# Kernel optimization log

Hardware: AMD Instinct MI355X
Metric: run time of the kernel (lower is better)

The kernel has to match this reference:

```python
import jax, jax.numpy as jnp
import numpy as np

B, L = 2, 4096
D_MODEL, STATE, CONV, EXPAND, HEADDIM = 1024, 128, 4, 2, 64
D_INNER = EXPAND * D_MODEL            # 2048
NHEADS = D_INNER // HEADDIM           # 32
CONV_DIM = D_INNER + 2 * STATE        # x, B, C channels (ngroups=1)
D_IN_PROJ = 2 * D_INNER + 2 * STATE + NHEADS
MLP_INNER = 4096
EPS = 1e-5

def _silu(x):
    return x * jax.nn.sigmoid(x)

def _rmsnorm_prenorm(x, res, w):
    # rmsnorm_fn(prenorm=True): residual update then RMSNorm of the residual
    res = x + res
    normed = res * jax.lax.rsqrt(jnp.mean(res * res, axis=-1, keepdims=True) + EPS)
    return normed * w, res

def _mamba2(x, in_proj_w, conv_w, conv_b, dt_bias, A_log, D_param, out_proj_w):
    b, l, _ = x.shape
    zxbcdt = x @ in_proj_w.T                                   # (b,l,D_IN_PROJ)
    z, xBC, dt = jnp.split(zxbcdt, [D_INNER, D_INNER + CONV_DIM], axis=-1)
    # causal depthwise conv1d + silu over [x, B, C]
    xp = jnp.pad(xBC, ((0, 0), (CONV - 1, 0), (0, 0)))
    conv = sum(xp[:, j:j + l, :] * conv_w[None, None, :, j] for j in range(CONV)) + conv_b
    xBC = _silu(conv)
    xh, Bm, Cm = jnp.split(xBC, [D_INNER, D_INNER + STATE], axis=-1)
    xh = xh.reshape(b, l, NHEADS, HEADDIM)                     # (b,l,h,p)
    dt = jax.nn.softplus(dt + dt_bias)                         # (b,l,h)
    A = -jnp.exp(A_log)                                        # (h,)

    def step(state, inp):
        x_t, B_t, C_t, dt_t = inp                              # (b,h,p),(b,n),(b,n),(b,h)
        dA = jnp.exp(dt_t * A)                                 # (b,h)
        state = state * dA[..., None, None] + jnp.einsum('bh,bhp,bn->bhpn', dt_t, x_t, B_t)
        y_t = jnp.einsum('bhpn,bn->bhp', state, C_t)
        return state, y_t

    xs = (xh.transpose(1, 0, 2, 3), Bm.transpose(1, 0, 2), Cm.transpose(1, 0, 2), dt.transpose(1, 0, 2))
    state0 = jnp.zeros((b, NHEADS, HEADDIM, STATE), dtype=x.dtype)
    _, y = jax.lax.scan(step, state0, xs)                      # y: (l,b,h,p)
    y = y.transpose(1, 0, 2, 3) + D_param[None, None, :, None] * xh
    y = y * _silu(z).reshape(b, l, NHEADS, HEADDIM)            # rmsnorm=False -> gate with silu(z)
    return y.reshape(b, l, D_INNER) @ out_proj_w.T

def _mlp(x, gate_w, up_w, down_w):
    return (_silu(x @ gate_w.T) * (x @ up_w.T)) @ down_w.T

def setup_inputs() -> dict:
    key = jax.random.key(0)
    ks = jax.random.split(key, 12)
    s = 0.02
    return {
        'hidden_states': jax.random.normal(ks[0], (B, L, D_MODEL), jnp.float32),
        'residual': jax.random.normal(ks[1], (B, L, D_MODEL), jnp.float32),
        'ssm_norm_w': jnp.ones((D_MODEL,), jnp.float32),
        'mlp_norm_w': jnp.ones((D_MODEL,), jnp.float32),
        'in_proj_w': jax.random.normal(ks[2], (D_IN_PROJ, D_MODEL), jnp.float32) * s,
        'conv_w': jax.random.normal(ks[3], (CONV_DIM, CONV), jnp.float32) * 0.1,
        'conv_b': jnp.zeros((CONV_DIM,), jnp.float32),
        'dt_bias': jax.random.uniform(ks[4], (NHEADS,), jnp.float32, -4.0, -1.0),
        'A_log': jnp.log(jax.random.uniform(ks[5], (NHEADS,), jnp.float32, 1.0, 16.0)),
        'D_param': jnp.ones((NHEADS,), jnp.float32),
        'out_proj_w': jax.random.normal(ks[6], (D_MODEL, D_INNER), jnp.float32) * s,
        'mlp_gate_w': jax.random.normal(ks[7], (MLP_INNER, D_MODEL), jnp.float32) * s,
        'mlp_up_w': jax.random.normal(ks[8], (MLP_INNER, D_MODEL), jnp.float32) * s,
        'mlp_down_w': jax.random.normal(ks[9], (D_MODEL, MLP_INNER), jnp.float32) * s,
    }

def reference(hidden_states, residual, ssm_norm_w, mlp_norm_w, in_proj_w, conv_w, conv_b,
              dt_bias, A_log, D_param, out_proj_w, mlp_gate_w, mlp_up_w, mlp_down_w):
    h, res = _rmsnorm_prenorm(hidden_states, residual, ssm_norm_w)
    h = _mamba2(h, in_proj_w, conv_w, conv_b, dt_bias, A_log, D_param, out_proj_w)
    h, res = _rmsnorm_prenorm(h, res, mlp_norm_w)
    h = _mlp(h, mlp_gate_w, mlp_up_w, mlp_down_w)
    return h, res
```

## Files before the change

kernel.cpp:

```cpp
#include <hip/hip_runtime.h>

typedef __bf16 bf16x8 __attribute__((ext_vector_type(8)));
typedef float  f32x4  __attribute__((ext_vector_type(4)));

#define GLOAD_LDS16(gp, lp) \
  __builtin_amdgcn_global_load_lds((const __attribute__((address_space(1))) void*)(gp), \
                                   (__attribute__((address_space(3))) void*)(lp), 16, 0, 0)

__device__ __forceinline__ unsigned short f2bf(float f) {
  unsigned u = __float_as_uint(f);
  u += 0x7fffu + ((u >> 16) & 1u);
  return (unsigned short)(u >> 16);
}
__device__ __forceinline__ float bf2f(unsigned short h) {
  return __uint_as_float(((unsigned)h) << 16);
}
__device__ __forceinline__ f32x4 splat4(float v) { f32x4 r = {v, v, v, v}; return r; }

__device__ __forceinline__ f32x4 up4(unsigned lo, unsigned hi) {
  f32x4 r;
  r[0] = __uint_as_float(lo << 16); r[1] = __uint_as_float(lo & 0xffff0000u);
  r[2] = __uint_as_float(hi << 16); r[3] = __uint_as_float(hi & 0xffff0000u);
  return r;
}
__device__ __forceinline__ unsigned pk2(float a, float b) {
  return (unsigned)f2bf(a) | ((unsigned)f2bf(b) << 16);
}

__device__ __forceinline__ void store_out(unsigned short* C, size_t idx, float v) {
  C[idx] = f2bf(v);
}
__device__ __forceinline__ void store_out(float* C, size_t idx, float v) {
  C[idx] = v;
}

__global__ __launch_bounds__(256) void rmsnorm1_kernel(
    const float* __restrict__ hid, const float* __restrict__ resin,
    const float* __restrict__ w, float* __restrict__ resout,
    unsigned short* __restrict__ hout)
{
  const int row = blockIdx.x, t = threadIdx.x;
  const size_t base = (size_t)row * 1024;
  float4 h = ((const float4*)(hid + base))[t];
  float4 r = ((const float4*)(resin + base))[t];
  float4 s; s.x = h.x + r.x; s.y = h.y + r.y; s.z = h.z + r.z; s.w = h.w + r.w;
  float ss = s.x*s.x + s.y*s.y + s.z*s.z + s.w*s.w;
  #pragma unroll
  for (int off = 32; off; off >>= 1) ss += __shfl_down(ss, off, 64);
  __shared__ float red[4];
  if ((t & 63) == 0) red[t >> 6] = ss;
  __syncthreads();
  float tot = red[0] + red[1] + red[2] + red[3];
  float sc = rsqrtf(tot * (1.0f/1024.0f) + 1e-5f);
  ((float4*)(resout + base))[t] = s;
  float4 wv = ((const float4*)w)[t];
  ushort4 o = make_ushort4(f2bf(s.x*sc*wv.x), f2bf(s.y*sc*wv.y),
                           f2bf(s.z*sc*wv.z), f2bf(s.w*sc*wv.w));
  ((ushort4*)(hout + base))[t] = o;
}

__global__ __launch_bounds__(256) void rmsnorm2_kernel(
    const unsigned short* __restrict__ mo, const float* __restrict__ res1,
    const float* __restrict__ w, float* __restrict__ res_out,
    unsigned short* __restrict__ h2)
{
  const int row = blockIdx.x, t = threadIdx.x;
  const size_t base = (size_t)row * 1024;
  float4 r = ((const float4*)(res1 + base))[t];
  ushort4 m = ((const ushort4*)(mo + base))[t];
  float4 s; s.x = r.x + bf2f(m.x); s.y = r.y + bf2f(m.y);
            s.z = r.z + bf2f(m.z); s.w = r.w + bf2f(m.w);
  float ss = s.x*s.x + s.y*s.y + s.z*s.z + s.w*s.w;
  #pragma unroll
  for (int off = 32; off; off >>= 1) ss += __shfl_down(ss, off, 64);
  __shared__ float red[4];
  if ((t & 63) == 0) red[t >> 6] = ss;
  __syncthreads();
  float tot = red[0] + red[1] + red[2] + red[3];
  float sc = rsqrtf(tot * (1.0f/1024.0f) + 1e-5f);
  ((float4*)(res_out + base))[t] = s;
  float4 wv = ((const float4*)w)[t];
  ((ushort4*)(h2 + base))[t] = make_ushort4(f2bf(s.x*sc*wv.x), f2bf(s.y*sc*wv.y),
                                            f2bf(s.z*sc*wv.z), f2bf(s.w*sc*wv.w));
}

__global__ __launch_bounds__(256) void cast_w(
    const float* __restrict__ src, unsigned short* __restrict__ dst,
    int rows, int cols, int prows)
{
  size_t i4 = ((size_t)blockIdx.x * 256 + threadIdx.x) * 4;
  size_t total = (size_t)prows * cols;
  if (i4 >= total) return;
  int r = (int)(i4 / cols);
  ushort4 o;
  if (r < rows) {
    float4 v = *(const float4*)(src + i4);
    o = make_ushort4(f2bf(v.x), f2bf(v.y), f2bf(v.z), f2bf(v.w));
  } else {
    o = make_ushort4(0, 0, 0, 0);
  }
  *(ushort4*)(dst + i4) = o;
}

template <typename OutT, int TN>
__global__ __launch_bounds__(512) void gemm256(
    const unsigned short* __restrict__ A, const unsigned short* __restrict__ W,
    OutT* __restrict__ C, int K, int lda, int ldc, int Nst)
{
  constexpr int NI = TN / 64;
  constexpr int WN = TN / 4;
  constexpr int SB = 2 + TN / 128;
  __shared__ unsigned short As[2][2][8192];
  __shared__ unsigned short Bs[2][2][TN * 32];

  const int gx = gridDim.x, nwg = gx * (int)gridDim.y;
  int lin = blockIdx.y * gx + blockIdx.x;
  {
    const int q = nwg >> 3, r = nwg & 7, xcd = lin & 7, lo = lin >> 3;
    lin = (xcd < r ? xcd * (q + 1) : r * (q + 1) + (xcd - r) * q) + lo;
  }
  const int n0 = (lin % gx) * TN, m0 = (lin / gx) << 8;

  const int t = threadIdx.x, lane = t & 63, w = t >> 6;
  const int wr = w >> 2, wc = w & 3;
  const int fr = lane & 15, fq = lane >> 4;
  const int gsw = ((fq ^ ((fr ^ (fr >> 2)) & 3)) << 3);
  const int srl = t >> 2;
  const int sg  = (t & 3);

  f32x4 acc[8][NI];
  #pragma unroll
  for (int i = 0; i < 8; ++i)
    #pragma unroll
    for (int j = 0; j < NI; ++j) acc[i][j] = splat4(0.f);

  auto stageA = [&](int buf, int ks, int kc) {
    #pragma unroll
    for (int h = 0; h < 2; ++h) {
      const int rl = h * 128 + srl;
      const int swz = (rl ^ (rl >> 2)) & 3;
      const unsigned short* g = A + (size_t)(m0 + rl) * lda + kc + ks * 32 + ((sg ^ swz) << 3);
      GLOAD_LDS16(g, &As[buf][ks][h * 4096 + (w << 9)]);
    }
  };
  auto stageB = [&](int buf, int ks, int kc) {
    #pragma unroll
    for (int h = 0; h < TN / 128; ++h) {
      const int rl = h * 128 + srl;
      const int swz = (rl ^ (rl >> 2)) & 3;
      const unsigned short* g = W + (size_t)(n0 + rl) * (size_t)K + kc + ks * 32 + ((sg ^ swz) << 3);
      GLOAD_LDS16(g, &Bs[buf][ks][h * 4096 + (w << 9)]);
    }
  };

  auto phase = [&](int cb, int ks) {
    bf16x8 af[8], bq[NI];
    #pragma unroll
    for (int mi = 0; mi < 8; ++mi) {
      const int R = wr * 128 + mi * 16 + fr;
      af[mi] = *(const bf16x8*)(&As[cb][ks][R * 32 + gsw]);
    }
    #pragma unroll
    for (int ni = 0; ni < NI; ++ni) {
      const int R = wc * WN + ni * 16 + fr;
      bq[ni] = *(const bf16x8*)(&Bs[cb][ks][R * 32 + gsw]);
    }
    __builtin_amdgcn_s_setprio(1);
    #pragma unroll
    for (int mi = 0; mi < 8; ++mi)
      #pragma unroll
      for (int ni = 0; ni < NI; ++ni)
        acc[mi][ni] = __builtin_amdgcn_mfma_f32_16x16x32_bf16(af[mi], bq[ni], acc[mi][ni], 0, 0, 0);
    __builtin_amdgcn_s_setprio(0);
  };

  stageA(0, 0, 0); stageB(0, 0, 0);
  stageA(0, 1, 0); stageB(0, 1, 0);

  const int NKT = K >> 6;
  for (int kt = 0; kt < NKT; ++kt) {
    const int cb = kt & 1, nb = cb ^ 1;
    const bool pre = (kt + 1 < NKT);
    const int kc = (kt + 1) << 6;
    if (pre) {
      stageA(nb, 0, kc); stageB(nb, 0, kc);
      asm volatile("s_waitcnt vmcnt(%0)" :: "n"(2 * SB) : "memory");
    } else {
      asm volatile("s_waitcnt vmcnt(%0)" :: "n"(SB) : "memory");
    }
    asm volatile("s_barrier" ::: "memory");
    phase(cb, 0);
    asm volatile("s_barrier" ::: "memory");
    if (pre) {
      stageA(nb, 1, kc); stageB(nb, 1, kc);
      asm volatile("s_waitcnt vmcnt(%0)" :: "n"(2 * SB) : "memory");
    } else {
      asm volatile("s_waitcnt vmcnt(0)" ::: "memory");
    }
    asm volatile("s_barrier" ::: "memory");
    phase(cb, 1);
    asm volatile("s_barrier" ::: "memory");
  }

  #pragma unroll
  for (int mi = 0; mi < 8; ++mi)
    #pragma unroll
    for (int ni = 0; ni < NI; ++ni)
      #pragma unroll
      for (int rr = 0; rr < 4; ++rr) {
        const int gm = m0 + wr * 128 + mi * 16 + fq * 4 + rr;
        const int gn = n0 + wc * WN + ni * 16 + fr;
        if (gn < Nst) store_out(C, (size_t)gm * ldc + gn, acc[mi][ni][rr]);
      }
}

__global__ __launch_bounds__(256) void conv_dt_kernel(
    const unsigned short* __restrict__ zx, const float* __restrict__ conv_w,
    const float* __restrict__ conv_b, const float* __restrict__ dt_bias,
    const float* __restrict__ A_log, unsigned short* __restrict__ conv_out,
    float2* __restrict__ dtda)
{
  size_t idx = (size_t)blockIdx.x * 256 + threadIdx.x;
  if (idx >= (size_t)8192 * 2336) return;
  int c = (int)(idx % 2336);
  int row = (int)(idx / 2336);
  int l = row & 4095;
  if (c < 2304) {
    float acc = conv_b[c];
    const float* wp = conv_w + c * 4;
    #pragma unroll
    for (int j = 0; j < 4; j++) {
      int ls = l - 3 + j;
      if (ls >= 0) acc += bf2f(zx[(size_t)(row - 3 + j) * 4480 + 2048 + c]) * wp[j];
    }
    float s = acc / (1.0f + expf(-acc));
    conv_out[(size_t)row * 2304 + c] = f2bf(s);
  } else {
    int h = c - 2304;
    float draw = bf2f(zx[(size_t)row * 4480 + 4352 + h]) + dt_bias[h];
    float sp = (draw > 20.0f) ? draw : log1pf(expf(draw));
    float Ah = -expf(A_log[h]);
    dtda[(size_t)row * 32 + h] = make_float2(sp, expf(sp * Ah));
  }
}


__global__ __launch_bounds__(256) void chunk_state_kernel(
    const unsigned short* __restrict__ convo, const float2* __restrict__ dtda,
    const float* __restrict__ A_log, unsigned short* __restrict__ Sg,
    float* __restrict__ Pend)
{
  __shared__ __align__(16) unsigned short bT[128 * 136];
  __shared__ __align__(16) unsigned short xT[64 * 136];
  __shared__ float wsh[128];
  const int t = threadIdx.x, lane = t & 63, wv = t >> 6;
  const int c = blockIdx.x & 31, h = (blockIdx.x >> 5) & 31, b = (int)(blockIdx.x >> 10);
  const size_t r0 = (size_t)b * 4096 + (size_t)c * 128;

  if (wv == 0) {
    const float A = -expf(A_log[h]);
    const float s0 = dtda[(r0 + 2 * lane) * 32 + h].x;
    const float s1 = dtda[(r0 + 2 * lane + 1) * 32 + h].x;
    const float v1 = s1 * A;
    float ps = s0 * A + v1;
    #pragma unroll
    for (int off = 1; off < 64; off <<= 1) {
      float n = __shfl_up(ps, off, 64);
      if (lane >= off) ps += n;
    }
    const float laQ = __shfl(ps, 63, 64);
    wsh[2 * lane]     = expf(laQ - (ps - v1)) * s0;
    wsh[2 * lane + 1] = expf(laQ - ps) * s1;
    if (lane == 63) Pend[blockIdx.x] = expf(laQ);
  }
  __syncthreads();

  {
    int j = t >> 3;
    const int p0 = (t & 7) << 3;
    #pragma unroll
    for (int it = 0; it < 4; ++it, j += 32) {
      const uint4 v = *(const uint4*)(convo + (r0 + j) * 2304 + h * 64 + p0);
      const float w = wsh[j];
      const unsigned arr[4] = {v.x, v.y, v.z, v.w};
      #pragma unroll
      for (int e = 0; e < 8; ++e) {
        const unsigned short raw = (unsigned short)(arr[e >> 1] >> ((e & 1) * 16));
        xT[(p0 + e) * 136 + j] = f2bf(bf2f(raw) * w);
      }
    }
  }
  {
    int j = t >> 4;
    const int n0 = (t & 15) << 3;
    #pragma unroll
    for (int it = 0; it < 8; ++it, j += 16) {
      const uint4 v = *(const uint4*)(convo + (r0 + j) * 2304 + 2048 + n0);
      const unsigned arr[4] = {v.x, v.y, v.z, v.w};
      #pragma unroll
      for (int e = 0; e < 8; ++e)
        bT[(n0 + e) * 136 + j] = (unsigned short)(arr[e >> 1] >> ((e & 1) * 16));
    }
  }
  __syncthreads();

  const int fr = lane & 15, fq = lane >> 4;
  const int wn = wv << 5;
  f32x4 acc[4][2];
  #pragma unroll
  for (int i = 0; i < 4; ++i)
    #pragma unroll
    for (int j = 0; j < 2; ++j) acc[i][j] = splat4(0.f);

  #pragma unroll
  for (int k0 = 0; k0 < 128; k0 += 32) {
    bf16x8 af[4], bf[2];
    #pragma unroll
    for (int i = 0; i < 4; ++i)
      af[i] = *(const bf16x8*)(xT + (i * 16 + fr) * 136 + fq * 8 + k0);
    #pragma unroll
    for (int j = 0; j < 2; ++j)
      bf[j] = *(const bf16x8*)(bT + (wn + j * 16 + fr) * 136 + fq * 8 + k0);
    #pragma unroll
    for (int i = 0; i < 4; ++i)
      #pragma unroll
      for (int j = 0; j < 2; ++j)
        acc[i][j] = __builtin_amdgcn_mfma_f32_16x16x32_bf16(af[i], bf[j], acc[i][j], 0, 0, 0);
  }

  const size_t slot = (size_t)blockIdx.x * 8192;
  #pragma unroll
  for (int i = 0; i < 4; ++i)
    #pragma unroll
    for (int j = 0; j < 2; ++j)
      #pragma unroll
      for (int r = 0; r < 4; ++r)
        Sg[slot + (size_t)(i * 16 + fq * 4 + r) * 128 + wn + j * 16 + fr] = f2bf(acc[i][j][r]);
}

__global__ __launch_bounds__(256) void chunk_combine_kernel(
    unsigned short* __restrict__ S, const float* __restrict__ Pend)
{
  const int t = threadIdx.x;
  const int sl = blockIdx.x & 7, bh = blockIdx.x >> 3;
  const size_t e = (size_t)sl * 1024 + (size_t)t * 4;
  f32x4 run = splat4(0.f);
  for (int c = 0; c < 32; ++c) {
    const size_t addr = (size_t)(bh * 32 + c) * 8192 + e;
    const uint2 a = *(const uint2*)(S + addr);
    const float P = Pend[bh * 32 + c];
    *(uint2*)(S + addr) = make_uint2(pk2(run[0], run[1]), pk2(run[2], run[3]));
    const f32x4 av = up4(a.x, a.y);
    run = av + splat4(P) * run;
  }
}

__global__ __launch_bounds__(256, 2) void chunk_output_kernel(
    unsigned short* __restrict__ convo, const float2* __restrict__ dtda,
    const float* __restrict__ A_log, const unsigned short* __restrict__ Sg,
    const unsigned short* __restrict__ zx, const float* __restrict__ D_param)
{
  __shared__ __align__(16) unsigned short bm[128 * 136];
  __shared__ __align__(16) unsigned short xT[64 * 136];
  __shared__ float la_s[128];
  __shared__ float dt_s[128];
  const int t = threadIdx.x, lane = t & 63, wv = t >> 6;
  const int c = blockIdx.x & 31, h = (blockIdx.x >> 5) & 31, b = (int)(blockIdx.x >> 10);
  const size_t r0 = (size_t)b * 4096 + (size_t)c * 128;

  if (wv == 0) {
    const float A = -expf(A_log[h]);
    const float s0 = dtda[(r0 + 2 * lane) * 32 + h].x;
    const float s1 = dtda[(r0 + 2 * lane + 1) * 32 + h].x;
    const float v1 = s1 * A;
    float ps = s0 * A + v1;
    #pragma unroll
    for (int off = 1; off < 64; off <<= 1) {
      float n = __shfl_up(ps, off, 64);
      if (lane >= off) ps += n;
    }
    la_s[2 * lane] = ps - v1;
    la_s[2 * lane + 1] = ps;
    dt_s[2 * lane] = s0;
    dt_s[2 * lane + 1] = s1;
  }

  {
    int j = t >> 4;
    const int n0 = (t & 15) << 3;
    #pragma unroll
    for (int it = 0; it < 8; ++it, j += 16)
      *(uint4*)(bm + j * 136 + n0) = *(const uint4*)(convo + (r0 + j) * 2304 + 2048 + n0);
  }
  {
    int j = t >> 3;
    const int p0 = (t & 7) << 3;
    #pragma unroll
    for (int it = 0; it < 4; ++it, j += 32) {
      const uint4 v = *(const uint4*)(convo + (r0 + j) * 2304 + h * 64 + p0);
      const unsigned arr[4] = {v.x, v.y, v.z, v.w};
      #pragma unroll
      for (int e = 0; e < 8; ++e)
        xT[(p0 + e) * 136 + j] = (unsigned short)(arr[e >> 1] >> ((e & 1) * 16));
    }
  }
  __syncthreads();

  const int fr = lane & 15, fq = lane >> 4;
  const int wm = wv << 5;
  const unsigned short* Cbase = convo + r0 * 2304 + 2176 + fq * 8;

  f32x4 acc_g[2][8];
  #pragma unroll
  for (int mt = 0; mt < 2; ++mt)
    #pragma unroll
    for (int nt = 0; nt < 8; ++nt) acc_g[mt][nt] = splat4(0.f);
  #pragma unroll
  for (int k0 = 0; k0 < 128; k0 += 32) {
    bf16x8 af[2], bg[8];
    #pragma unroll
    for (int mt = 0; mt < 2; ++mt)
      af[mt] = *(const bf16x8*)(Cbase + (size_t)(wm + mt * 16 + fr) * 2304 + k0);
    #pragma unroll
    for (int nt = 0; nt < 8; ++nt)
      bg[nt] = *(const bf16x8*)(bm + (nt * 16 + fr) * 136 + fq * 8 + k0);
    #pragma unroll
    for (int mt = 0; mt < 2; ++mt)
      #pragma unroll
      for (int nt = 0; nt < 8; ++nt)
        acc_g[mt][nt] = __builtin_amdgcn_mfma_f32_16x16x32_bf16(af[mt], bg[nt], acc_g[mt][nt], 0, 0, 0);
  }
  __syncthreads();

  #pragma unroll
  for (int mt = 0; mt < 2; ++mt)
    #pragma unroll
    for (int r = 0; r < 4; ++r) {
      const int i = wm + mt * 16 + fq * 4 + r;
      const float lai = la_s[i];
      #pragma unroll
      for (int nt = 0; nt < 8; ++nt) {
        const int j = nt * 16 + fr;
        float v = 0.f;
        if (j <= i) v = acc_g[mt][nt][r] * expf(lai - la_s[j]) * dt_s[j];
        bm[i * 136 + j] = f2bf(v);
      }
    }

  const size_t slot = (size_t)blockIdx.x * 8192;
  f32x4 acc_y[2][4];
  #pragma unroll
  for (int mt = 0; mt < 2; ++mt)
    #pragma unroll
    for (int pt = 0; pt < 4; ++pt) acc_y[mt][pt] = splat4(0.f);
  #pragma unroll
  for (int k0 = 0; k0 < 128; k0 += 32) {
    bf16x8 af[2], bs[4];
    #pragma unroll
    for (int mt = 0; mt < 2; ++mt)
      af[mt] = *(const bf16x8*)(Cbase + (size_t)(wm + mt * 16 + fr) * 2304 + k0);
    #pragma unroll
    for (int pt = 0; pt < 4; ++pt)
      bs[pt] = *(const bf16x8*)(Sg + slot + (size_t)(pt * 16 + fr) * 128 + fq * 8 + k0);
    #pragma unroll
    for (int mt = 0; mt < 2; ++mt)
      #pragma unroll
      for (int pt = 0; pt < 4; ++pt)
        acc_y[mt][pt] = __builtin_amdgcn_mfma_f32_16x16x32_bf16(af[mt], bs[pt], acc_y[mt][pt], 0, 0, 0);
  }
  #pragma unroll
  for (int mt = 0; mt < 2; ++mt)
    #pragma unroll
    for (int r = 0; r < 4; ++r) {
      const float el = expf(la_s[wm + mt * 16 + fq * 4 + r]);
      #pragma unroll
      for (int pt = 0; pt < 4; ++pt) acc_y[mt][pt][r] *= el;
    }
  __syncthreads();

  #pragma unroll
  for (int k0 = 0; k0 < 128; k0 += 32) {
    bf16x8 am[2], bx[4];
    #pragma unroll
    for (int mt = 0; mt < 2; ++mt)
      am[mt] = *(const bf16x8*)(bm + (wm + mt * 16 + fr) * 136 + fq * 8 + k0);
    #pragma unroll
    for (int pt = 0; pt < 4; ++pt)
      bx[pt] = *(const bf16x8*)(xT + (pt * 16 + fr) * 136 + fq * 8 + k0);
    #pragma unroll
    for (int mt = 0; mt < 2; ++mt)
      #pragma unroll
      for (int pt = 0; pt < 4; ++pt)
        acc_y[mt][pt] = __builtin_amdgcn_mfma_f32_16x16x32_bf16(am[mt], bx[pt], acc_y[mt][pt], 0, 0, 0);
  }

  const float D = D_param[h];
  #pragma unroll
  for (int mt = 0; mt < 2; ++mt)
    #pragma unroll
    for (int r = 0; r < 4; ++r) {
      const int i = wm + mt * 16 + fq * 4 + r;
      const size_t grow = r0 + i;
      #pragma unroll
      for (int pt = 0; pt < 4; ++pt) {
        const int p = pt * 16 + fr;
        const float x = bf2f(xT[p * 136 + i]);
        const float z = bf2f(zx[grow * 4480 + h * 64 + p]);
        const float sg = z / (1.0f + expf(-z));
        convo[grow * 2304 + h * 64 + p] = f2bf((acc_y[mt][pt][r] + D * x) * sg);
      }
    }
}

__global__ __launch_bounds__(256) void act_kernel(
    unsigned short* __restrict__ g, const unsigned short* __restrict__ u)
{
  size_t i4 = ((size_t)blockIdx.x * 256 + threadIdx.x) * 4;
  if (i4 >= (size_t)8192 * 4096) return;
  ushort4 gv = *(ushort4*)(g + i4);
  ushort4 uv = *(const ushort4*)(u + i4);
  float x, s, o[4];
  x = bf2f(gv.x); s = x / (1.0f + expf(-x)); o[0] = s * bf2f(uv.x);
  x = bf2f(gv.y); s = x / (1.0f + expf(-x)); o[1] = s * bf2f(uv.y);
  x = bf2f(gv.z); s = x / (1.0f + expf(-x)); o[2] = s * bf2f(uv.z);
  x = bf2f(gv.w); s = x / (1.0f + expf(-x)); o[3] = s * bf2f(uv.w);
  *(ushort4*)(g + i4) = make_ushort4(f2bf(o[0]), f2bf(o[1]), f2bf(o[2]), f2bf(o[3]));
}

static constexpr size_t OFF_RES1 = 0;
static constexpr size_t OFF_H1   = 33554432;
static constexpr size_t OFF_W    = 83886080;
static constexpr size_t OFF_ZX   = 93061120;
static constexpr size_t OFF_CONV = 166461440;
static constexpr size_t OFF_DTDA = 204210176;
static constexpr size_t OFF_U    = 0;

extern "C" void kernel_launch(void* const* d_in, const int* in_sizes, int n_in,
                              void* d_out, int out_size, void* d_ws, size_t ws_size,
                              hipStream_t stream) {
  const float* hid      = (const float*)d_in[0];
  const float* resid    = (const float*)d_in[1];
  const float* ssm_w    = (const float*)d_in[2];
  const float* mlp_w    = (const float*)d_in[3];
  const float* in_proj  = (const float*)d_in[4];
  const float* conv_w   = (const float*)d_in[5];
  const float* conv_b   = (const float*)d_in[6];
  const float* dt_bias  = (const float*)d_in[7];
  const float* A_log    = (const float*)d_in[8];
  const float* D_param  = (const float*)d_in[9];
  const float* out_proj = (const float*)d_in[10];
  const float* gate_w   = (const float*)d_in[11];
  const float* up_w     = (const float*)d_in[12];
  const float* down_w   = (const float*)d_in[13];
  float* out = (float*)d_out;
  char* ws = (char*)d_ws;

  float*          res1  = (float*)(ws + OFF_RES1);
  unsigned short* h1    = (unsigned short*)(ws + OFF_H1);
  unsigned short* Wb    = (unsigned short*)(ws + OFF_W);
  unsigned short* zx    = (unsigned short*)(ws + OFF_ZX);
  unsigned short* convo = (unsigned short*)(ws + OFF_CONV);
  float2*         dtda  = (float2*)(ws + OFF_DTDA);
  unsigned short* ub    = (unsigned short*)(ws + OFF_U);
  unsigned short* Sg    = h1;
  float*          Pend  = (float*)(ws + OFF_W);
  unsigned short* WinP  = convo;

  rmsnorm1_kernel<<<8192, 256, 0, stream>>>(hid, resid, ssm_w, res1, h1);
  cast_w<<<4608, 256, 0, stream>>>(in_proj, WinP, 4384, 1024, 4608);
  gemm256<unsigned short, 256><<<dim3(18, 32), 512, 0, stream>>>(h1, WinP, zx, 1024, 1024, 4480, 4480);
  conv_dt_kernel<<<74752, 256, 0, stream>>>(zx, conv_w, conv_b, dt_bias, A_log,
                                            convo, dtda);
  chunk_state_kernel<<<2048, 256, 0, stream>>>(convo, dtda, A_log, Sg, Pend);
  chunk_combine_kernel<<<512, 256, 0, stream>>>(Sg, Pend);
  chunk_output_kernel<<<2048, 256, 0, stream>>>(convo, dtda, A_log, Sg, zx, D_param);
  cast_w<<<2048, 256, 0, stream>>>(out_proj, Wb, 1024, 2048, 1024);
  gemm256<unsigned short, 128><<<dim3(8, 32), 512, 0, stream>>>(convo, Wb, h1, 2048, 2304, 1024, 1024);
  rmsnorm2_kernel<<<8192, 256, 0, stream>>>(h1, res1, mlp_w, out + 8388608, convo);
  cast_w<<<4096, 256, 0, stream>>>(gate_w, Wb, 4096, 1024, 4096);
  gemm256<unsigned short, 256><<<dim3(16, 32), 512, 0, stream>>>(convo, Wb, zx, 1024, 1024, 4096, 4096);
  cast_w<<<4096, 256, 0, stream>>>(up_w, Wb, 4096, 1024, 4096);
  gemm256<unsigned short, 256><<<dim3(16, 32), 512, 0, stream>>>(convo, Wb, ub, 1024, 1024, 4096, 4096);
  act_kernel<<<32768, 256, 0, stream>>>(zx, ub);
  cast_w<<<4096, 256, 0, stream>>>(down_w, Wb, 1024, 4096, 1024);
  gemm256<float, 128><<<dim3(8, 32), 512, 0, stream>>>(zx, Wb, out, 4096, 4096, 1024, 1024);
}
```

Before: 928.9 us.

## Restructure bf16 GEMM main loop into four-quadrant ping-pong with staggered prefetch

Changes the LDS tiles to hold a 64-wide K slice per row with an 8-way XOR swizzle, replacing the two 32-wide K sub-tiles. Each K tile is now split into four MFMA quadrants (two M halves by two N halves). Global-to-LDS loads for the next tiles are spread between those quadrants, and A is prefetched two tiles ahead. B fragments are reused across quadrants and there are explicit lgkmcnt waits and sched barriers. The aim is to overlap memory traffic with MFMA work and reduce LDS bank conflicts, at the cost of more barriers per K tile and hardcoded vmcnt accounting.

Result: faster. 877.5 us (-5.5%).

```diff
diff --git a/kernel.cpp b/kernel.cpp
--- a/kernel.cpp
+++ b/kernel.cpp
@@ -107,11 +107,11 @@
     const unsigned short* __restrict__ A, const unsigned short* __restrict__ W,
     OutT* __restrict__ C, int K, int lda, int ldc, int Nst)
 {
-  constexpr int NI = TN / 64;
+  constexpr int NH = TN / 128;
   constexpr int WN = TN / 4;
-  constexpr int SB = 2 + TN / 128;
-  __shared__ unsigned short As[2][2][8192];
-  __shared__ unsigned short Bs[2][2][TN * 32];
+  constexpr int QN = TN / 128;
+  __shared__ __align__(16) unsigned short As[2][2][8192];
+  __shared__ __align__(16) unsigned short Bs[2][NH][8192];
 
   const int gx = gridDim.x, nwg = gx * (int)gridDim.y;
   int lin = blockIdx.y * gx + blockIdx.x;
@@ -124,93 +124,119 @@
   const int t = threadIdx.x, lane = t & 63, w = t >> 6;
   const int wr = w >> 2, wc = w & 3;
   const int fr = lane & 15, fq = lane >> 4;
-  const int gsw = ((fq ^ ((fr ^ (fr >> 2)) & 3)) << 3);
-  const int srl = t >> 2;
-  const int sg  = (t & 3);
-
-  f32x4 acc[8][NI];
+
+  f32x4 acc[8][2 * QN];
   #pragma unroll
   for (int i = 0; i < 8; ++i)
     #pragma unroll
-    for (int j = 0; j < NI; ++j) acc[i][j] = splat4(0.f);
-
-  auto stageA = [&](int buf, int ks, int kc) {
-    #pragma unroll
-    for (int h = 0; h < 2; ++h) {
-      const int rl = h * 128 + srl;
-      const int swz = (rl ^ (rl >> 2)) & 3;
-      const unsigned short* g = A + (size_t)(m0 + rl) * lda + kc + ks * 32 + ((sg ^ swz) << 3);
-      GLOAD_LDS16(g, &As[buf][ks][h * 4096 + (w << 9)]);
+    for (int j = 0; j < 2 * QN; ++j) acc[i][j] = splat4(0.f);
+
+  auto stA = [&](int buf, int h, int kc) {
+    #pragma unroll
+    for (int r2 = 0; r2 < 2; ++r2) {
+      const int R = r2 * 64 + (t >> 3);
+      const unsigned short* g =
+          A + (size_t)(m0 + h * 128 + R) * lda + kc + (((t & 7) ^ (R & 7)) << 3);
+      GLOAD_LDS16(g, &As[buf][h][r2 * 4096 + t * 8]);
     }
   };
-  auto stageB = [&](int buf, int ks, int kc) {
-    #pragma unroll
-    for (int h = 0; h < TN / 128; ++h) {
-      const int rl = h * 128 + srl;
-      const int swz = (rl ^ (rl >> 2)) & 3;
-      const unsigned short* g = W + (size_t)(n0 + rl) * (size_t)K + kc + ks * 32 + ((sg ^ swz) << 3);
-      GLOAD_LDS16(g, &Bs[buf][ks][h * 4096 + (w << 9)]);
+  auto stB = [&](int buf, int h, int kc) {
+    #pragma unroll
+    for (int r2 = 0; r2 < 2; ++r2) {
+      const int R = r2 * 64 + (t >> 3);
+      const unsigned short* g =
+          W + (size_t)(n0 + h * 128 + R) * (size_t)K + kc + (((t & 7) ^ (R & 7)) << 3);
+      GLOAD_LDS16(g, &Bs[buf][h][r2 * 4096 + t * 8]);
     }
   };
 
-  auto phase = [&](int cb, int ks) {
-    bf16x8 af[8], bq[NI];
-    #pragma unroll
-    for (int mi = 0; mi < 8; ++mi) {
-      const int R = wr * 128 + mi * 16 + fr;
-      af[mi] = *(const bf16x8*)(&As[cb][ks][R * 32 + gsw]);
-    }
-    #pragma unroll
-    for (int ni = 0; ni < NI; ++ni) {
-      const int R = wc * WN + ni * 16 + fr;
-      bq[ni] = *(const bf16x8*)(&Bs[cb][ks][R * 32 + gsw]);
-    }
-    __builtin_amdgcn_s_setprio(1);
-    #pragma unroll
-    for (int mi = 0; mi < 8; ++mi)
-      #pragma unroll
-      for (int ni = 0; ni < NI; ++ni)
-        acc[mi][ni] = __builtin_amdgcn_mfma_f32_16x16x32_bf16(af[mi], bq[ni], acc[mi][ni], 0, 0, 0);
-    __builtin_amdgcn_s_setprio(0);
-  };
-
-  stageA(0, 0, 0); stageB(0, 0, 0);
-  stageA(0, 1, 0); stageB(0, 1, 0);
+  bf16x8 af[4][2], bqX[QN][2], bqY[QN][2];
+
+#define G256_LDA(MH)                                                           \
+  _Pragma("unroll") for (int mi = 0; mi < 4; ++mi)                             \
+    _Pragma("unroll") for (int ks = 0; ks < 2; ++ks) {                         \
+      const int R = (MH) * 64 + mi * 16 + fr;                                  \
+      af[mi][ks] = *(const bf16x8*)(&As[cb][wr][R * 64 +                       \
+                        ((((ks << 2) + fq) ^ (R & 7)) << 3)]);                 \
+    }
+
+#define G256_LDB(BQ, NHH)                                                      \
+  _Pragma("unroll") for (int ni = 0; ni < QN; ++ni)                            \
+    _Pragma("unroll") for (int ks = 0; ks < 2; ++ks) {                         \
+      const int half = (NH == 2) ? (wc >> 1) : 0;                              \
+      const int R = (NH == 2) ? ((wc & 1) * 64 + (NHH) * 32 + ni * 16 + fr)    \
+                              : (wc * 32 + (NHH) * 16 + fr);                   \
+      BQ[ni][ks] = *(const bf16x8*)(&Bs[cb][half][R * 64 +                     \
+                        ((((ks << 2) + fq) ^ (R & 7)) << 3)]);                 \
+    }
+
+#define G256_WAITL                                                             \
+  asm volatile("s_waitcnt lgkmcnt(0)" ::: "memory");                           \
+  __builtin_amdgcn_sched_barrier(0);
+
+#define G256_MQ(BQ, MH, NHH)                                                   \
+  __builtin_amdgcn_s_setprio(1);                                               \
+  _Pragma("unroll") for (int ks = 0; ks < 2; ++ks)                             \
+    _Pragma("unroll") for (int mi = 0; mi < 4; ++mi)                           \
+      _Pragma("unroll") for (int ni = 0; ni < QN; ++ni)                        \
+        acc[(MH) * 4 + mi][(NHH) * QN + ni] =                                  \
+            __builtin_amdgcn_mfma_f32_16x16x32_bf16(                           \
+                af[mi][ks], BQ[ni][ks],                                        \
+                acc[(MH) * 4 + mi][(NHH) * QN + ni], 0, 0, 0);                 \
+  __builtin_amdgcn_s_setprio(0);
 
   const int NKT = K >> 6;
+  stA(0, 0, 0);
+  stB(0, 0, 0);
+  stA(0, 1, 0);
+  if (NH > 1) stB(0, 1, 0);
+  if (NKT > 1) stA(1, 0, 64);
+
   for (int kt = 0; kt < NKT; ++kt) {
     const int cb = kt & 1, nb = cb ^ 1;
-    const bool pre = (kt + 1 < NKT);
-    const int kc = (kt + 1) << 6;
-    if (pre) {
-      stageA(nb, 0, kc); stageB(nb, 0, kc);
-      asm volatile("s_waitcnt vmcnt(%0)" :: "n"(2 * SB) : "memory");
-    } else {
-      asm volatile("s_waitcnt vmcnt(%0)" :: "n"(SB) : "memory");
-    }
-    asm volatile("s_barrier" ::: "memory");
-    phase(cb, 0);
-    asm volatile("s_barrier" ::: "memory");
-    if (pre) {
-      stageA(nb, 1, kc); stageB(nb, 1, kc);
-      asm volatile("s_waitcnt vmcnt(%0)" :: "n"(2 * SB) : "memory");
+    const int kc1 = (kt + 1) << 6, kc2 = (kt + 2) << 6;
+    const bool p1 = (kt + 1 < NKT), p2 = (kt + 2 < NKT);
+    if (p1) {
+      stB(nb, 0, kc1); stA(nb, 1, kc1);
+      asm volatile("s_waitcnt vmcnt(6)" ::: "memory");
     } else {
       asm volatile("s_waitcnt vmcnt(0)" ::: "memory");
     }
-    asm volatile("s_barrier" ::: "memory");
-    phase(cb, 1);
-    asm volatile("s_barrier" ::: "memory");
-  }
+    __builtin_amdgcn_s_barrier();
+    G256_LDA(0)
+    G256_LDB(bqX, 0)
+    G256_WAITL
+    G256_MQ(bqX, 0, 0)
+    __builtin_amdgcn_s_barrier();
+    if (NH > 1 && p1) stB(nb, 1, kc1);
+    G256_LDB(bqY, 1)
+    G256_WAITL
+    G256_MQ(bqY, 0, 1)
+    __builtin_amdgcn_s_barrier();
+    G256_LDA(1)
+    G256_WAITL
+    G256_MQ(bqY, 1, 1)
+    __builtin_amdgcn_s_barrier();
+    if (p2) stA(cb, 0, kc2);
+    G256_LDB(bqX, 0)
+    G256_WAITL
+    G256_MQ(bqX, 1, 0)
+    __builtin_amdgcn_s_barrier();
+  }
+#undef G256_LDA
+#undef G256_LDB
+#undef G256_WAITL
+#undef G256_MQ
 
   #pragma unroll
   for (int mi = 0; mi < 8; ++mi)
     #pragma unroll
-    for (int ni = 0; ni < NI; ++ni)
+    for (int ci = 0; ci < 2 * QN; ++ci)
       #pragma unroll
       for (int rr = 0; rr < 4; ++rr) {
         const int gm = m0 + wr * 128 + mi * 16 + fq * 4 + rr;
-        const int gn = n0 + wc * WN + ni * 16 + fr;
-        if (gn < Nst) store_out(C, (size_t)gm * ldc + gn, acc[mi][ni][rr]);
+        const int gn = n0 + wc * WN + ci * 16 + fr;
+        if (gn < Nst) store_out(C, (size_t)gm * ldc + gn, acc[mi][ci][rr]);
       }
 }
 
```
